# Kernel optimization log

Hardware: AMD Instinct MI355X
Metric: run time of the kernel (lower is better)

Reference implementation:

```python
import jax, jax.numpy as jnp
import numpy as np

N, DIM, H, D, S, B = 30000, 256, 8, 64, 32, 8
INNER = H * D


def setup_inputs() -> dict:
    key = jax.random.key(0)
    ks = jax.random.split(key, 16)
    def w(k, shape, fan_in):
        return jax.random.normal(k, shape, dtype=jnp.float32) / np.sqrt(fan_in)
    x = jax.random.normal(ks[0], (N, DIM), dtype=jnp.float32)
    batch = jnp.sort(jax.random.randint(ks[1], (N,), 0, B))
    return {
        'x': x,
        'batch': batch,
        'W_fx': w(ks[2], (DIM, INNER), DIM), 'b_fx': jnp.zeros((INNER,), jnp.float32),
        'W_x': w(ks[3], (DIM, INNER), DIM), 'b_x': jnp.zeros((INNER,), jnp.float32),
        'W_slice': w(ks[4], (D, S), D), 'b_slice': jnp.zeros((S,), jnp.float32),
        'graph_temp': 0.5 * jnp.ones((1, H, 1), jnp.float32),
        'W_q': w(ks[5], (D, D), D), 'W_k': w(ks[6], (D, D), D), 'W_v': w(ks[7], (D, D), D),
        'W_out': w(ks[8], (INNER, DIM), INNER), 'b_out': jnp.zeros((DIM,), jnp.float32),
    }


def reference(x, batch, W_fx, b_fx, W_x, b_x, W_slice, b_slice, graph_temp,
              W_q, W_k, W_v, W_out, b_out):
    n = x.shape[0]
    scale = D ** -0.5
    fx = (x @ W_fx + b_fx).reshape(n, H, D)   # [N,H,D]
    xm = (x @ W_x + b_x).reshape(n, H, D)     # [N,H,D]
    # per-node slice assignment weights, tempered softmax over slices
    logits = (jnp.einsum('nhd,ds->nhs', xm, W_slice) + b_slice) / graph_temp
    w = jax.nn.softmax(logits, axis=-1)       # [N,H,S]
    onehot = jax.nn.one_hot(batch, B, dtype=x.dtype)  # [N,B]
    # scatter-add pooling per graph: slice_norm[b,h,s], slice_token[b,h,s,d]
    slice_norm = jax.ops.segment_sum(w, batch, num_segments=B)  # [B,H,S]
    wb = w[:, None, :, :] * onehot[:, :, None, None]            # [N,B,H,S]
    slice_token = jnp.einsum('nbhs,nhd->bhsd', wb, fx)
    slice_token = slice_token / (slice_norm[..., None] + 1e-5)
    # small attention over slice tokens
    q = jnp.einsum('bhsd,de->bhse', slice_token, W_q)
    k = jnp.einsum('bhsd,de->bhse', slice_token, W_k)
    v = jnp.einsum('bhsd,de->bhse', slice_token, W_v)
    attn = jax.nn.softmax(jnp.einsum('bhsd,bhtd->bhst', q, k) * scale, axis=-1)
    out_tok = jnp.einsum('bhst,bhtd->bhsd', attn, v)            # [B,H,S,D]
    # gather back to nodes with weighted reduction over slices
    tmp = jnp.einsum('nhs,bhsd->nbhd', w, out_tok)              # [N,B,H,D]
    out_x = jnp.einsum('nb,nbhd->nhd', onehot, tmp).reshape(n, INNER)
    return out_x @ W_out + b_out
```

## Files before the change

### kernel.cpp

```cpp
#include <hip/hip_runtime.h>

#define NDIM 256
#define INNER 512
#define NH 8
#define ND 64
#define NS 32
#define NB 8
#define NP 30208

typedef __attribute__((ext_vector_type(8))) short short8;
typedef __attribute__((ext_vector_type(4))) float f32x4;

static __device__ __forceinline__ short f2bf(float f) {
  unsigned u = __float_as_uint(f);
  unsigned r = (u + 0x7fffu + ((u >> 16) & 1u)) >> 16;
  return (short)r;
}
static __device__ __forceinline__ float bf2f(short s) {
  return __uint_as_float(((unsigned)(unsigned short)s) << 16);
}

static __device__ __forceinline__ void gl_lds16(const void* g, void* l) {
  __builtin_amdgcn_global_load_lds(
      (const __attribute__((address_space(1))) unsigned int*)g,
      (__attribute__((address_space(3))) unsigned int*)l, 16, 0, 0);
}

__global__ __launch_bounds__(256) void k_xsplit(
    const float* __restrict__ x, short* __restrict__ Xh, short* __restrict__ Xl,
    int total4)
{
  int id = blockIdx.x * 256 + threadIdx.x;
  if (id >= total4) return;
  float4 v = *(const float4*)&x[(size_t)id * 4];
  short h0 = f2bf(v.x), h1 = f2bf(v.y), h2 = f2bf(v.z), h3 = f2bf(v.w);
  short4 hv = make_short4(h0, h1, h2, h3);
  short4 lv = make_short4(f2bf(v.x - bf2f(h0)), f2bf(v.y - bf2f(h1)),
                          f2bf(v.z - bf2f(h2)), f2bf(v.w - bf2f(h3)));
  *(short4*)&Xh[(size_t)id * 4] = hv;
  *(short4*)&Xl[(size_t)id * 4] = lv;
}

__global__ __launch_bounds__(256) void k_prep(
    const float* __restrict__ Wfx, const float* __restrict__ Wx,
    const float* __restrict__ bx, const float* __restrict__ Wsl,
    const float* __restrict__ bsl,
    short* __restrict__ Bt1h, short* __restrict__ Bt1l,
    float* __restrict__ bcomb, int* __restrict__ seg)
{
  int id = blockIdx.x * 256 + threadIdx.x;
  if (id < 131072) {
    int k = id >> 9, n = id & 511;
    float v = Wfx[k * 512 + n];
    short hi = f2bf(v); short lo = f2bf(v - bf2f(hi));
    Bt1h[n * 256 + k] = hi; Bt1l[n * 256 + k] = lo;
  } else if (id < 196608) {
    int e = id - 131072;
    int c = e & 255, k = e >> 8;
    int h = c >> 5, s = c & 31;
    float acc = 0.f;
    #pragma unroll 8
    for (int d = 0; d < 64; d++) acc += Wx[k * 512 + h * 64 + d] * Wsl[d * 32 + s];
    short hi = f2bf(acc); short lo = f2bf(acc - bf2f(hi));
    Bt1h[(512 + c) * 256 + k] = hi; Bt1l[(512 + c) * 256 + k] = lo;
  } else if (id < 196864) {
    int c = id - 196608;
    int h = c >> 5, s = c & 31;
    float acc = bsl[s];
    #pragma unroll 8
    for (int d = 0; d < 64; d++) acc += bx[h * 64 + d] * Wsl[d * 32 + s];
    bcomb[c] = acc;
  } else if (id < 196880) {
    int v = id - 196864;
    seg[v] = (v == 0) ? 0 : 0x7fffffff;
  }
}

__global__ __launch_bounds__(256) void k_segs(
    const int* __restrict__ batch, int* __restrict__ seg, int N)
{
  int i = blockIdx.x * 256 + threadIdx.x;
  if (i >= N) return;
  int b = batch[i];
  int p = (i == 0) ? -1 : batch[i - 1];
  for (int v = p + 1; v <= b; v++)
    if (v >= 1) atomicMin(&seg[v], i);
  if (i == N - 1)
    for (int v = b + 1; v <= 8; v++) atomicMin(&seg[v], N);
}

__global__ __launch_bounds__(512, 4) void k_fxw(
    const short* __restrict__ Xh, const short* __restrict__ Xl,
    const short* __restrict__ Bt1h, const short* __restrict__ Bt1l,
    const float* __restrict__ bfx, const float* __restrict__ bcomb,
    const float* __restrict__ gtemp,
    short* __restrict__ fxTh, short* __restrict__ fxTl,
    short* __restrict__ wh_out, short* __restrict__ wl_out,
    int N, int ntiles)
{
  __shared__ __align__(16) short smem[17408];
  short* AhL = &smem[0];
  short* AlL = &smem[4096];
  short* BhL = &smem[8192];
  short* BlL = &smem[12288];

  const int lid = blockIdx.x;
  const int xcd = lid & 7;
  const int idx = lid >> 3;
  const int ct  = idx % 6;
  const int rowt = xcd + 8 * (idx / 6);
  if (rowt >= ntiles) return;
  const int row0 = rowt * 128;
  const int tid = threadIdx.x;
  const int lane = tid & 63, l15 = lane & 15, quad = lane >> 4;
  const int wvi = tid >> 6;
  const int wm = wvi & 1, wn = wvi >> 1;
  const int ctbase = ct * 128;
  const int srow = lane & 15, schunk = lane >> 4;

  f32x4 acc[4][2];
  #pragma unroll
  for (int i = 0; i < 4; i++)
    #pragma unroll
    for (int j = 0; j < 2; j++) acc[i][j] = (f32x4){0.f, 0.f, 0.f, 0.f};

  for (int kt = 0; kt < 8; kt++) {
    {
      int gr = row0 + wvi * 16 + srow;
      if (gr > N - 1) gr = N - 1;
      size_t aoff = (size_t)gr * 256 + kt * 32 + schunk * 8;
      int br = ctbase + wvi * 16 + srow;
      size_t boff = (size_t)br * 256 + kt * 32 + schunk * 8;
      gl_lds16(Xh + aoff, AhL + wvi * 512);
      gl_lds16(Xl + aoff, AlL + wvi * 512);
      gl_lds16(Bt1h + boff, BhL + wvi * 512);
      gl_lds16(Bt1l + boff, BlL + wvi * 512);
    }
    __syncthreads();

    short8 ah[4], al[4];
    #pragma unroll
    for (int mt = 0; mt < 4; mt++) {
      int rg = wm * 4 + mt;
      ah[mt] = *(const short8*)&AhL[rg * 512 + quad * 128 + l15 * 8];
      al[mt] = *(const short8*)&AlL[rg * 512 + quad * 128 + l15 * 8];
    }
    #pragma unroll
    for (int nt = 0; nt < 2; nt++) {
      int rg = wn * 2 + nt;
      short8 bh = *(const short8*)&BhL[rg * 512 + quad * 128 + l15 * 8];
      short8 bl = *(const short8*)&BlL[rg * 512 + quad * 128 + l15 * 8];
      #pragma unroll
      for (int mt = 0; mt < 4; mt++) {
        acc[mt][nt] = __builtin_amdgcn_mfma_f32_16x16x32_bf16(ah[mt], bh, acc[mt][nt], 0, 0, 0);
        acc[mt][nt] = __builtin_amdgcn_mfma_f32_16x16x32_bf16(ah[mt], bl, acc[mt][nt], 0, 0, 0);
        acc[mt][nt] = __builtin_amdgcn_mfma_f32_16x16x32_bf16(al[mt], bh, acc[mt][nt], 0, 0, 0);
      }
    }
    __syncthreads();
  }

  if (ct < 4) {
    short (*T)[136] = (short(*)[136])&smem[0];
    #pragma unroll
    for (int pass = 0; pass < 2; pass++) {
      __syncthreads();
      #pragma unroll
      for (int nt = 0; nt < 2; nt++) {
        int cl = wn * 32 + nt * 16 + l15;
        float bias = bfx[ctbase + cl];
        #pragma unroll
        for (int mt = 0; mt < 4; mt++)
          #pragma unroll
          for (int r = 0; r < 4; r++) {
            int rl = wm * 64 + mt * 16 + quad * 4 + r;
            float v = acc[mt][nt][r] + bias;
            short hi2 = f2bf(v);
            T[cl][rl] = pass ? f2bf(v - bf2f(hi2)) : hi2;
          }
      }
      __syncthreads();
      short* dst = pass ? fxTl : fxTh;
      #pragma unroll
      for (int t = 0; t < 4; t++) {
        int idx2 = tid + t * 512;
        int row = idx2 >> 4, kc = (idx2 & 15) * 8;
        *(int4*)&dst[(size_t)(ctbase + row) * NP + row0 + kc] = *(const int4*)&T[row][kc];
      }
    }
  } else {
    int ct2 = ct - 4;
    int lcbase = ct2 * 128 + wn * 32;
    int h = lcbase >> 5;
    float inv_t = 1.0f / gtemp[h];
    int lc0 = lcbase + l15, lc1 = lcbase + 16 + l15;
    float b0 = bcomb[lc0], b1 = bcomb[lc1];
    #pragma unroll
    for (int mt = 0; mt < 4; mt++) {
      #pragma unroll
      for (int r = 0; r < 4; r++) {
        float s0 = (acc[mt][0][r] + b0) * inv_t;
        float s1 = (acc[mt][1][r] + b1) * inv_t;
        float m = fmaxf(s0, s1);
        #pragma unroll
        for (int off = 1; off < 16; off <<= 1) m = fmaxf(m, __shfl_xor(m, off, 16));
        float e0 = __expf(s0 - m), e1 = __expf(s1 - m);
        float sum = e0 + e1;
        #pragma unroll
        for (int off = 1; off < 16; off <<= 1) sum += __shfl_xor(sum, off, 16);
        float inv = 1.0f / sum;
        int row = row0 + wm * 64 + mt * 16 + quad * 4 + r;
        if (row < N) {
          float w0v = e0 * inv, w1v = e1 * inv;
          size_t base = (size_t)row * (NH * NS);
          short h0 = f2bf(w0v), h1 = f2bf(w1v);
          wh_out[base + lc0] = h0; wl_out[base + lc0] = f2bf(w0v - bf2f(h0));
          wh_out[base + lc1] = h1; wl_out[base + lc1] = f2bf(w1v - bf2f(h1));
        }
      }
    }
  }
}

__global__ __launch_bounds__(256) void k_scat(
    const short* __restrict__ wh, const short* __restrict__ wl,
    const short* __restrict__ fxTh, const short* __restrict__ fxTl,
    const int* __restrict__ seg,
    float* __restrict__ stok, float* __restrict__ snorm, int N)
{
  __shared__ short wth[32][136];
  __shared__ short wtl[32][136];
  __shared__ short fh[64][136];
  __shared__ short fl[64][136];
  __shared__ float ln[32];

  const int h = blockIdx.y;
  const int n0 = blockIdx.x * 512;
  const int tid = threadIdx.x;
  const int lane = tid & 63, l15 = lane & 15, quad = lane >> 4;
  const int wv = tid >> 6;
  const int nend = min(n0 + 512, N);

  f32x4 acc0 = (f32x4){0.f, 0.f, 0.f, 0.f};
  f32x4 acc1 = (f32x4){0.f, 0.f, 0.f, 0.f};

  for (int b = 0; b < NB; b++) {
    int lo = max(seg[b], n0), hi = min(seg[b + 1], nend);
    if (lo >= hi) continue;
    if (tid < 32) ln[tid] = 0.f;
    int c0lo = (lo - n0) & ~127;
    int c0hi = hi - n0;
    for (int c0 = c0lo; c0 < c0hi; c0 += 128) {
      __syncthreads();
      #pragma unroll
      for (int t = 0; t < 2; t++) {
        int idx2 = tid + t * 256;
        int row = idx2 >> 2;
        int sc  = (idx2 & 3) * 8;
        int ng = n0 + c0 + row;
        short8 vh = (short8){0,0,0,0,0,0,0,0};
        short8 vl = (short8){0,0,0,0,0,0,0,0};
        if (ng >= lo && ng < hi) {
          size_t src = (size_t)ng * 256 + h * 32 + sc;
          vh = *(const short8*)&wh[src];
          vl = *(const short8*)&wl[src];
        }
        #pragma unroll
        for (int j = 0; j < 8; j++) {
          wth[sc + j][row] = vh[j];
          wtl[sc + j][row] = vl[j];
        }
      }
      #pragma unroll
      for (int t = 0; t < 4; t++) {
        int idx2 = tid + t * 256;
        int row = idx2 >> 4, kc = (idx2 & 15) * 8;
        size_t src = (size_t)(h * 64 + row) * NP + n0 + c0 + kc;
        *(int4*)&fh[row][kc] = *(const int4*)&fxTh[src];
        *(int4*)&fl[row][kc] = *(const int4*)&fxTl[src];
      }
      __syncthreads();

      {
        int s = tid >> 3, g = tid & 7;
        float sum = 0.f;
        #pragma unroll
        for (int i2 = 0; i2 < 16; i2++) {
          int nl = g * 16 + i2;
          sum += bf2f(wth[s][nl]) + bf2f(wtl[s][nl]);
        }
        atomicAdd(&ln[s], sum);
      }

      for (int k0 = 0; k0 < 128; k0 += 32) {
        int gbase = n0 + c0 + k0;
        if (gbase + 32 <= lo || gbase >= hi) continue;
        short8 a0h = *(const short8*)&wth[l15][k0 + quad * 8];
        short8 a0l = *(const short8*)&wtl[l15][k0 + quad * 8];
        short8 a1h = *(const short8*)&wth[16 + l15][k0 + quad * 8];
        short8 a1l = *(const short8*)&wtl[16 + l15][k0 + quad * 8];
        short8 bh = *(const short8*)&fh[wv * 16 + l15][k0 + quad * 8];
        short8 bl = *(const short8*)&fl[wv * 16 + l15][k0 + quad * 8];
        acc0 = __builtin_amdgcn_mfma_f32_16x16x32_bf16(a0h, bh, acc0, 0, 0, 0);
        acc0 = __builtin_amdgcn_mfma_f32_16x16x32_bf16(a0h, bl, acc0, 0, 0, 0);
        acc0 = __builtin_amdgcn_mfma_f32_16x16x32_bf16(a0l, bh, acc0, 0, 0, 0);
        acc1 = __builtin_amdgcn_mfma_f32_16x16x32_bf16(a1h, bh, acc1, 0, 0, 0);
        acc1 = __builtin_amdgcn_mfma_f32_16x16x32_bf16(a1h, bl, acc1, 0, 0, 0);
        acc1 = __builtin_amdgcn_mfma_f32_16x16x32_bf16(a1l, bh, acc1, 0, 0, 0);
      }
    }
    __syncthreads();
    size_t base = ((size_t)b * NH + h) * NS;
    #pragma unroll
    for (int r = 0; r < 4; r++) {
      atomicAdd(&stok[(base + quad * 4 + r) * ND + wv * 16 + l15], acc0[r]);
      atomicAdd(&stok[(base + 16 + quad * 4 + r) * ND + wv * 16 + l15], acc1[r]);
    }
    if (tid < 32) atomicAdd(&snorm[base + tid], ln[tid]);
    acc0 = (f32x4){0.f, 0.f, 0.f, 0.f};
    acc1 = (f32x4){0.f, 0.f, 0.f, 0.f};
    __syncthreads();
  }
}

__global__ __launch_bounds__(256) void k_attn(
    const float* __restrict__ stok, const float* __restrict__ snorm,
    const float* __restrict__ Wq, const float* __restrict__ Wk,
    const float* __restrict__ Wv, const float* __restrict__ Wout,
    short* __restrict__ PTh, short* __restrict__ PTl)
{
  __shared__ __align__(16) float st[32][68];
  __shared__ __align__(16) float qs[32][68];
  __shared__ __align__(16) float ks[32][68];
  __shared__ __align__(16) float vs[32][68];
  __shared__ __align__(16) float at[32][36];
  __shared__ __align__(16) float ot[32][68];
  __shared__ __align__(16) float wo[64][256];

  const int bh = blockIdx.x;
  const int b = bh >> 3, h = bh & 7;
  const int tid = threadIdx.x;
  const int lane = tid & 63;
  const int wv = tid >> 6;

  {
    const float* wsrc = Wout + (size_t)h * 16384;
    float* wdst = &wo[0][0];
    #pragma unroll
    for (int r = 0; r < 16; r++) {
      int off = r * 1024 + wv * 256;
      gl_lds16(wsrc + off + lane * 4, wdst + off);
    }
  }

  for (int i = tid; i < 2048; i += 256) {
    int ss = i >> 6, dd = i & 63;
    float nrm = snorm[(size_t)bh * NS + ss] + 1e-5f;
    st[ss][dd] = stok[(size_t)bh * 2048 + i] / nrm;
  }
  __syncthreads();

  {
    float aq[8], ak[8], av[8];
    #pragma unroll
    for (int i = 0; i < 8; i++) { aq[i] = 0.f; ak[i] = 0.f; av[i] = 0.f; }
    for (int ch = 0; ch < 16; ch++) {
      float4 sv[8];
      #pragma unroll
      for (int i = 0; i < 8; i++) sv[i] = *(const float4*)&st[wv * 8 + i][ch * 4];
      #pragma unroll
      for (int d = 0; d < 4; d++) {
        int dd = ch * 4 + d;
        float wq = Wq[dd * 64 + lane];
        float wk = Wk[dd * 64 + lane];
        float wvv = Wv[dd * 64 + lane];
        #pragma unroll
        for (int i = 0; i < 8; i++) {
          float sd = (d == 0) ? sv[i].x : (d == 1) ? sv[i].y : (d == 2) ? sv[i].z : sv[i].w;
          aq[i] = fmaf(sd, wq, aq[i]);
          ak[i] = fmaf(sd, wk, ak[i]);
          av[i] = fmaf(sd, wvv, av[i]);
        }
      }
    }
    #pragma unroll
    for (int i = 0; i < 8; i++) {
      qs[wv * 8 + i][lane] = aq[i];
      ks[wv * 8 + i][lane] = ak[i];
      vs[wv * 8 + i][lane] = av[i];
    }
  }
  __syncthreads();

  {
    const int si = tid >> 3, tj0 = (tid & 7) * 4;
    float a0 = 0.f, a1 = 0.f, a2 = 0.f, a3 = 0.f;
    for (int ch = 0; ch < 16; ch++) {
      float4 q4 = *(const float4*)&qs[si][ch * 4];
      float4 k0 = *(const float4*)&ks[tj0 + 0][ch * 4];
      float4 k1 = *(const float4*)&ks[tj0 + 1][ch * 4];
      float4 k2 = *(const float4*)&ks[tj0 + 2][ch * 4];
      float4 k3 = *(const float4*)&ks[tj0 + 3][ch * 4];
      a0 += q4.x * k0.x + q4.y * k0.y + q4.z * k0.z + q4.w * k0.w;
      a1 += q4.x * k1.x + q4.y * k1.y + q4.z * k1.z + q4.w * k1.w;
      a2 += q4.x * k2.x + q4.y * k2.y + q4.z * k2.z + q4.w * k2.w;
      a3 += q4.x * k3.x + q4.y * k3.y + q4.z * k3.z + q4.w * k3.w;
    }
    const float scale = 0.125f;
    *(float4*)&at[si][tj0] = (float4){a0 * scale, a1 * scale, a2 * scale, a3 * scale};
  }
  __syncthreads();

  {
    const int row = tid >> 3, jb = (tid & 7) * 4;
    float4 v = *(const float4*)&at[row][jb];
    float m = fmaxf(fmaxf(v.x, v.y), fmaxf(v.z, v.w));
    #pragma unroll
    for (int off = 1; off < 8; off <<= 1) m = fmaxf(m, __shfl_xor(m, off, 8));
    float e0 = __expf(v.x - m), e1 = __expf(v.y - m);
    float e2 = __expf(v.z - m), e3 = __expf(v.w - m);
    float s = e0 + e1 + e2 + e3;
    #pragma unroll
    for (int off = 1; off < 8; off <<= 1) s += __shfl_xor(s, off, 8);
    float inv = 1.f / s;
    *(float4*)&at[row][jb] = (float4){e0 * inv, e1 * inv, e2 * inv, e3 * inv};
  }
  __syncthreads();

  {
    float acc[8];
    #pragma unroll
    for (int i = 0; i < 8; i++) acc[i] = 0.f;
    for (int ch = 0; ch < 8; ch++) {
      float v0 = vs[ch * 4 + 0][lane];
      float v1 = vs[ch * 4 + 1][lane];
      float v2 = vs[ch * 4 + 2][lane];
      float v3 = vs[ch * 4 + 3][lane];
      #pragma unroll
      for (int i = 0; i < 8; i++) {
        float4 a4 = *(const float4*)&at[wv * 8 + i][ch * 4];
        acc[i] += a4.x * v0 + a4.y * v1 + a4.z * v2 + a4.w * v3;
      }
    }
    #pragma unroll
    for (int i = 0; i < 8; i++) ot[wv * 8 + i][lane] = acc[i];
  }
  __syncthreads();

  {
    const int c0 = 4 * (lane & 31) + 128 * (lane >> 5);
    float pacc[8][4];
    #pragma unroll
    for (int i = 0; i < 8; i++)
      #pragma unroll
      for (int c = 0; c < 4; c++) pacc[i][c] = 0.f;

    for (int ch = 0; ch < 16; ch++) {
      float4 w0 = *(const float4*)&wo[ch * 4 + 0][c0];
      float4 w1 = *(const float4*)&wo[ch * 4 + 1][c0];
      float4 w2 = *(const float4*)&wo[ch * 4 + 2][c0];
      float4 w3 = *(const float4*)&wo[ch * 4 + 3][c0];
      #pragma unroll
      for (int i = 0; i < 8; i++) {
        float4 o4 = *(const float4*)&ot[wv * 8 + i][ch * 4];
        pacc[i][0] = fmaf(o4.x, w0.x, pacc[i][0]);
        pacc[i][1] = fmaf(o4.x, w0.y, pacc[i][1]);
        pacc[i][2] = fmaf(o4.x, w0.z, pacc[i][2]);
        pacc[i][3] = fmaf(o4.x, w0.w, pacc[i][3]);
        pacc[i][0] = fmaf(o4.y, w1.x, pacc[i][0]);
        pacc[i][1] = fmaf(o4.y, w1.y, pacc[i][1]);
        pacc[i][2] = fmaf(o4.y, w1.z, pacc[i][2]);
        pacc[i][3] = fmaf(o4.y, w1.w, pacc[i][3]);
        pacc[i][0] = fmaf(o4.z, w2.x, pacc[i][0]);
        pacc[i][1] = fmaf(o4.z, w2.y, pacc[i][1]);
        pacc[i][2] = fmaf(o4.z, w2.z, pacc[i][2]);
        pacc[i][3] = fmaf(o4.z, w2.w, pacc[i][3]);
        pacc[i][0] = fmaf(o4.w, w3.x, pacc[i][0]);
        pacc[i][1] = fmaf(o4.w, w3.y, pacc[i][1]);
        pacc[i][2] = fmaf(o4.w, w3.z, pacc[i][2]);
        pacc[i][3] = fmaf(o4.w, w3.w, pacc[i][3]);
      }
    }

    #pragma unroll
    for (int cc = 0; cc < 4; cc++) {
      short8 hv, lv;
      #pragma unroll
      for (int i = 0; i < 8; i++) {
        float val = pacc[i][cc];
        short hi = f2bf(val);
        hv[i] = hi;
        lv[i] = f2bf(val - bf2f(hi));
      }
      size_t dst = ((size_t)b * NDIM + (c0 + cc)) * 256 + h * 32 + wv * 8;
      *(short8*)&PTh[dst] = hv;
      *(short8*)&PTl[dst] = lv;
    }
  }
}

__global__ __launch_bounds__(256) void k_outw(
    const short* __restrict__ wh, const short* __restrict__ wl,
    const short* __restrict__ PTh, const short* __restrict__ PTl,
    const int* __restrict__ batch, const float* __restrict__ bout,
    float* __restrict__ out, int N)
{
  __shared__ short Ah[128][40];
  __shared__ short Al[128][40];
  __shared__ short Bh[128][40];
  __shared__ short Bl[128][40];
  __shared__ int b_sh[128];

  const int ct = blockIdx.x;
  const int row0 = blockIdx.y * 128;
  const int tid = threadIdx.x;
  const int lane = tid & 63, l15 = lane & 15, quad = lane >> 4;
  const int wv = tid >> 6, wm = wv & 1, wn = wv >> 1;
  const int ctbase = ct * 128;
  const int cnt = min(128, N - row0);

  if (tid < 128) b_sh[tid] = (tid < cnt) ? batch[row0 + tid] : -1;
  __syncthreads();

  f32x4 acc[4][4];
  #pragma unroll
  for (int i = 0; i < 4; i++)
    #pragma unroll
    for (int j = 0; j < 4; j++) acc[i][j] = (f32x4){0.f, 0.f, 0.f, 0.f};

  int i0 = 0;
  while (i0 < cnt) {
    int b = b_sh[i0];
    int j = i0;
    while (j < cnt && b_sh[j] == b) j++;

    for (int kt = 0; kt < 8; kt++) {
      #pragma unroll
      for (int t = 0; t < 2; t++) {
        int i = tid + t * 256;
        int row = i >> 2, kc = (i & 3) * 8;
        int4 vh = make_int4(0, 0, 0, 0), vl = make_int4(0, 0, 0, 0);
        if (row >= i0 && row < j) {
          size_t src = (size_t)(row0 + row) * 256 + kt * 32 + kc;
          vh = *(const int4*)&wh[src];
          vl = *(const int4*)&wl[src];
        }
        *(int4*)&Ah[row][kc] = vh;
        *(int4*)&Al[row][kc] = vl;
      }
      #pragma unroll
      for (int t = 0; t < 2; t++) {
        int i = tid + t * 256;
        int row = i >> 2, kc = (i & 3) * 8;
        size_t src = ((size_t)b * NDIM + ctbase + row) * 256 + kt * 32 + kc;
        *(int4*)&Bh[row][kc] = *(const int4*)&PTh[src];
        *(int4*)&Bl[row][kc] = *(const int4*)&PTl[src];
      }
      __syncthreads();

      short8 ah[4], al[4];
      #pragma unroll
      for (int mt = 0; mt < 4; mt++) {
        int m = wm * 64 + mt * 16 + l15;
        ah[mt] = *(const short8*)&Ah[m][quad * 8];
        al[mt] = *(const short8*)&Al[m][quad * 8];
      }
      #pragma unroll
      for (int nt = 0; nt < 4; nt++) {
        int n = wn * 64 + nt * 16 + l15;
        short8 bh = *(const short8*)&Bh[n][quad * 8];
        short8 bl = *(const short8*)&Bl[n][quad * 8];
        #pragma unroll
        for (int mt = 0; mt < 4; mt++) {
          acc[mt][nt] = __builtin_amdgcn_mfma_f32_16x16x32_bf16(ah[mt], bh, acc[mt][nt], 0, 0, 0);
          acc[mt][nt] = __builtin_amdgcn_mfma_f32_16x16x32_bf16(ah[mt], bl, acc[mt][nt], 0, 0, 0);
          acc[mt][nt] = __builtin_amdgcn_mfma_f32_16x16x32_bf16(al[mt], bh, acc[mt][nt], 0, 0, 0);
        }
      }
      __syncthreads();
    }
    i0 = j;
  }

  #pragma unroll
  for (int nt = 0; nt < 4; nt++) {
    int c = ctbase + wn * 64 + nt * 16 + l15;
    float bias = bout[c];
    #pragma unroll
    for (int mt = 0; mt < 4; mt++)
      #pragma unroll
      for (int r = 0; r < 4; r++) {
        int row = row0 + wm * 64 + mt * 16 + quad * 4 + r;
        if (row < N) out[(size_t)row * NDIM + c] = acc[mt][nt][r] + bias;
      }
  }
}

extern "C" void kernel_launch(void* const* d_in, const int* in_sizes, int n_in,
                              void* d_out, int out_size, void* d_ws, size_t ws_size,
                              hipStream_t stream) {
  const float* x      = (const float*)d_in[0];
  const int*   batch  = (const int*)d_in[1];
  const float* Wfx    = (const float*)d_in[2];
  const float* bfx    = (const float*)d_in[3];
  const float* Wx     = (const float*)d_in[4];
  const float* bx     = (const float*)d_in[5];
  const float* Wsl    = (const float*)d_in[6];
  const float* bsl    = (const float*)d_in[7];
  const float* gtemp  = (const float*)d_in[8];
  const float* Wq     = (const float*)d_in[9];
  const float* Wk     = (const float*)d_in[10];
  const float* Wv     = (const float*)d_in[11];
  const float* Wout   = (const float*)d_in[12];
  const float* bout   = (const float*)d_in[13];
  float* out = (float*)d_out;

  const int N = in_sizes[0] / NDIM;

  float* stok  = (float*)d_ws;
  float* snorm = stok + 131072;
  float* bcomb = snorm + 2048;
  int*   seg   = (int*)(bcomb + 256);
  short* Bt1h  = (short*)(seg + 16);
  short* Bt1l  = Bt1h + 196608;
  short* Xh    = Bt1l + 196608;
  short* Xl    = Xh + 7680000;
  short* whb   = Xl + 7680000;
  short* wlb   = whb + (size_t)NP * 256;
  short* fxTh  = wlb + (size_t)NP * 256;
  short* fxTl  = fxTh + (size_t)512 * NP;
  short* PTh   = fxTl + (size_t)512 * NP;
  short* PTl   = PTh + 524288;

  hipMemsetAsync(stok, 0, (size_t)(131072 + 2048) * sizeof(float), stream);

  k_xsplit<<<(N * 64 + 255) / 256, 256, 0, stream>>>(x, Xh, Xl, N * 64);

  k_prep<<<770, 256, 0, stream>>>(Wfx, Wx, bx, Wsl, bsl, Bt1h, Bt1l, bcomb, seg);

  k_segs<<<(N + 255) / 256, 256, 0, stream>>>(batch, seg, N);

  const int ntiles = (N + 127) / 128;
  const int qmax = (ntiles + 7) / 8;
  k_fxw<<<8 * qmax * 6, 512, 0, stream>>>(Xh, Xl, Bt1h, Bt1l, bfx, bcomb, gtemp,
                                          fxTh, fxTl, whb, wlb, N, ntiles);

  dim3 g2((N + 511) / 512, NH);
  k_scat<<<g2, 256, 0, stream>>>(whb, wlb, fxTh, fxTl, seg, stok, snorm, N);

  k_attn<<<NB * NH, 256, 0, stream>>>(stok, snorm, Wq, Wk, Wv, Wout, PTh, PTl);

  dim3 g5(2, (N + 127) / 128);
  k_outw<<<g5, 256, 0, stream>>>(whb, wlb, PTh, PTl, batch, bout, out, N);
}
```

Measured before the change: 269.7 us.

## Double-buffer LDS staging in k_fxw GEMM to overlap loads with MFMA

The K loop of the fused projection GEMM now uses two LDS buffers: the next k-tile is issued via global_load_lds before computing on the current one, with explicit vmcnt waits and raw barriers replacing __syncthreads. The aim is to hide global-load latency behind the MFMA work. LDS use grows from about 34KB to 64KB per block, which may cut occupancy below the launch-bounds target of 4 blocks per CU.

```diff
diff --git a/kernel.cpp b/kernel.cpp
--- a/kernel.cpp
+++ b/kernel.cpp
@@ -98,11 +98,7 @@
     short* __restrict__ wh_out, short* __restrict__ wl_out,
     int N, int ntiles)
 {
-  __shared__ __align__(16) short smem[17408];
-  short* AhL = &smem[0];
-  short* AlL = &smem[4096];
-  short* BhL = &smem[8192];
-  short* BlL = &smem[12288];
+  __shared__ __align__(16) short smem[32768];
 
   const int lid = blockIdx.x;
   const int xcd = lid & 7;
@@ -124,19 +120,37 @@
     #pragma unroll
     for (int j = 0; j < 2; j++) acc[i][j] = (f32x4){0.f, 0.f, 0.f, 0.f};
 
+  int gr = row0 + wvi * 16 + srow;
+  if (gr > N - 1) gr = N - 1;
+  const int br = ctbase + wvi * 16 + srow;
+  const size_t abase = (size_t)gr * 256 + schunk * 8;
+  const size_t bbase = (size_t)br * 256 + schunk * 8;
+
+#define STAGE(p, kt_) do {                                         \
+    short* base_ = &smem[(p) * 16384];                             \
+    gl_lds16(Xh + abase + (kt_) * 32, base_ + wvi * 512);          \
+    gl_lds16(Xl + abase + (kt_) * 32, base_ + 4096 + wvi * 512);   \
+    gl_lds16(Bt1h + bbase + (kt_) * 32, base_ + 8192 + wvi * 512); \
+    gl_lds16(Bt1l + bbase + (kt_) * 32, base_ + 12288 + wvi * 512);\
+  } while (0)
+
+  STAGE(0, 0);
+
+  #pragma unroll
   for (int kt = 0; kt < 8; kt++) {
-    {
-      int gr = row0 + wvi * 16 + srow;
-      if (gr > N - 1) gr = N - 1;
-      size_t aoff = (size_t)gr * 256 + kt * 32 + schunk * 8;
-      int br = ctbase + wvi * 16 + srow;
-      size_t boff = (size_t)br * 256 + kt * 32 + schunk * 8;
-      gl_lds16(Xh + aoff, AhL + wvi * 512);
-      gl_lds16(Xl + aoff, AlL + wvi * 512);
-      gl_lds16(Bt1h + boff, BhL + wvi * 512);
-      gl_lds16(Bt1l + boff, BlL + wvi * 512);
-    }
-    __syncthreads();
+    if (kt < 7) {
+      STAGE((kt + 1) & 1, kt + 1);
+      asm volatile("s_waitcnt vmcnt(4)" ::: "memory");
+    } else {
+      asm volatile("s_waitcnt vmcnt(0)" ::: "memory");
+    }
+    __builtin_amdgcn_s_barrier();
+    asm volatile("" ::: "memory");
+
+    const short* AhL = &smem[(kt & 1) * 16384];
+    const short* AlL = AhL + 4096;
+    const short* BhL = AhL + 8192;
+    const short* BlL = AhL + 12288;
 
     short8 ah[4], al[4];
     #pragma unroll
@@ -157,8 +171,11 @@
         acc[mt][nt] = __builtin_amdgcn_mfma_f32_16x16x32_bf16(al[mt], bh, acc[mt][nt], 0, 0, 0);
       }
     }
-    __syncthreads();
-  }
+
+    asm volatile("s_waitcnt lgkmcnt(0)" ::: "memory");
+    __builtin_amdgcn_s_barrier();
+  }
+#undef STAGE
 
   if (ct < 4) {
     short (*T)[136] = (short(*)[136])&smem[0];
```

Result: no change. 266.5 us (median of 2 runs) (-1.2%).
